# Optimization experiments

Measured on AMD Instinct MI355X. Metric: run time of the kernel, lower is better.

Reference implementation:

```python
import jax, jax.numpy as jnp
import numpy as np

B, L, C_IN = 16, 512, 32
D_MODEL, D_STATE, D_CONV, EXPAND, PRED_LEN = 128, 16, 4, 2, 96
D_INNER = EXPAND * D_MODEL          # 256
DT_RANK = (D_MODEL + 15) // 16      # 8 (ceil(d_model/16), mamba_ssm default)


def setup_inputs() -> dict:
    key = jax.random.key(0)
    ks = jax.random.split(key, 14)
    f32 = jnp.float32
    nrm = lambda k, shape, sc: jax.random.normal(k, shape, f32) * sc
    inp = {
        "x": jax.random.normal(ks[0], (B, L, C_IN), f32),
        # input_proj: Linear(enc_in, d_model)
        "W_in": nrm(ks[1], (C_IN, D_MODEL), C_IN ** -0.5),
        "b_in": jnp.zeros((D_MODEL,), f32),
        # Mamba in_proj: Linear(d_model, 2*d_inner, bias=False)
        "W_inproj": nrm(ks[2], (D_MODEL, 2 * D_INNER), D_MODEL ** -0.5),
        # depthwise causal conv1d (d_inner, d_conv) + bias
        "conv_w": nrm(ks[3], (D_INNER, D_CONV), D_CONV ** -0.5),
        "conv_b": jnp.zeros((D_INNER,), f32),
        # x_proj: Linear(d_inner, dt_rank + 2*d_state, bias=False)
        "W_xproj": nrm(ks[4], (D_INNER, DT_RANK + 2 * D_STATE), D_INNER ** -0.5),
        # dt_proj: Linear(dt_rank, d_inner) with bias init so softplus(bias) ~ 1e-3..1e-1
        "W_dt": nrm(ks[5], (DT_RANK, D_INNER), DT_RANK ** -0.5),
        "b_dt": jax.random.uniform(ks[6], (D_INNER,), f32, minval=-6.0, maxval=-3.0),
        # S4D-real A init: A = -exp(A_log), A_log = log(1..d_state)
        "A_log": jnp.log(jnp.tile(jnp.arange(1, D_STATE + 1, dtype=f32), (D_INNER, 1))),
        "D": jnp.ones((D_INNER,), f32),
        # Mamba out_proj: Linear(d_inner, d_model, bias=False)
        "W_out": nrm(ks[7], (D_INNER, D_MODEL), D_INNER ** -0.5),
        # output_proj: Linear(d_model*seq_len, pred_len*enc_in)
        "W_outproj": nrm(ks[8], (D_MODEL * L, PRED_LEN * C_IN), (D_MODEL * L) ** -0.5),
        "b_outproj": jnp.zeros((PRED_LEN * C_IN,), f32),
    }
    return inp


def _mamba_forward(x, W_in, b_in, W_inproj, conv_w, conv_b, W_xproj,
                   W_dt, b_dt, A_log, D, W_out, W_outproj, b_outproj):
    Bb, Ll, Cc = x.shape
    d_inner, d_conv = conv_w.shape
    d_state = A_log.shape[1]
    dt_rank = W_dt.shape[0]

    h = x @ W_in + b_in                                  # (B,L,d_model)
    xz = h @ W_inproj                                    # (B,L,2*d_inner)
    u, z = jnp.split(xz, 2, axis=-1)                     # each (B,L,d_inner)

    # causal depthwise conv1d along L
    uc = jnp.transpose(u, (0, 2, 1))                     # (B,d_inner,L)
    kern = conv_w[:, None, :]                            # (d_inner,1,d_conv)
    uc = jax.lax.conv_general_dilated(
        uc, kern, window_strides=(1,), padding=[(d_conv - 1, 0)],
        dimension_numbers=("NCH", "OIH", "NCH"), feature_group_count=d_inner)
    u = jax.nn.silu(jnp.transpose(uc, (0, 2, 1)) + conv_b)   # (B,L,d_inner)

    # input-dependent dt, B, C
    xdbc = u @ W_xproj                                   # (B,L,dt_rank+2*d_state)
    dt = jax.nn.softplus(xdbc[..., :dt_rank] @ W_dt + b_dt)  # (B,L,d_inner)
    Bm = xdbc[..., dt_rank:dt_rank + d_state]            # (B,L,d_state)
    Cm = xdbc[..., dt_rank + d_state:]                   # (B,L,d_state)

    A = -jnp.exp(A_log)                                  # (d_inner,d_state)
    dA = jnp.exp(jnp.einsum('bld,dn->bldn', dt, A))      # discretized A
    dBu = jnp.einsum('bld,bln,bld->bldn', dt, Bm, u)     # discretized B*u

    def step(hstate, inputs):
        dA_t, dBu_t, C_t = inputs                        # (B,d,n),(B,d,n),(B,n)
        hstate = dA_t * hstate + dBu_t
        y_t = jnp.einsum('bdn,bn->bd', hstate, C_t)
        return hstate, y_t

    h0 = jnp.zeros((Bb, d_inner, d_state), u.dtype)
    _, ys = jax.lax.scan(step, h0, (jnp.moveaxis(dA, 1, 0),
                                    jnp.moveaxis(dBu, 1, 0),
                                    jnp.moveaxis(Cm, 1, 0)))
    y = jnp.moveaxis(ys, 0, 1) + u * D                   # (B,L,d_inner)
    y = y * jax.nn.silu(z)                               # gating
    m_out = y @ W_out                                    # (B,L,d_model)

    flat = m_out.reshape(Bb, -1)                         # (B, L*d_model)
    pred = flat @ W_outproj + b_outproj                  # (B, pred_len*enc_in)
    return pred.reshape(Bb, W_outproj.shape[1] // Cc, Cc)


def reference(x, W_in, b_in, W_inproj, conv_w, conv_b, W_xproj,
              W_dt, b_dt, A_log, D, W_out, W_outproj, b_outproj):
    return _mamba_forward(x, W_in, b_in, W_inproj, conv_w, conv_b, W_xproj,
                          W_dt, b_dt, A_log, D, W_out, W_outproj, b_outproj)
```

## Files before the change

### kernel.cpp

```cpp
#include <hip/hip_runtime.h>
#include <math.h>

#define NB 16
#define LL 512
#define CIN 32
#define DM 128
#define DS 16
#define DI 256
#define DTR 8
#define NCOL 3072
#define KTOT 65536
#define ROWS 8192
#define CH 64
#define CLEN 8
#define KC 512
#define KS 128
#define OUTSZ 49152

typedef float f32x2 __attribute__((ext_vector_type(2)));

__device__ __forceinline__ float sigmoidf_(float x){ return 1.f/(1.f+expf(-x)); }
__device__ __forceinline__ float softplusf_(float x){ return (x > 20.f) ? x : log1pf(expf(x)); }

__global__ void __launch_bounds__(256) k_A(
    const float* __restrict__ x, const float* __restrict__ W_in,
    const float* __restrict__ b_in, const float* __restrict__ W_ip,
    const float* __restrict__ cw, const float* __restrict__ cb,
    float* __restrict__ u, float* __restrict__ z) {
  __shared__ float xs[11][32];
  __shared__ float hs[11][128];
  __shared__ float up[11][256];
  int t = threadIdx.x;
  int b  = blockIdx.x >> 6;
  int lt = blockIdx.x & 63;
  int l0 = lt * 8;
  for (int i=t; i<11*32; i+=256) {
    int r = i >> 5, c = i & 31;
    int li = l0 - 3 + r;
    xs[r][c] = (li >= 0) ? x[((b<<9)+li)*CIN + c] : 0.f;
  }
  __syncthreads();
  for (int i=t; i<11*128; i+=256) {
    int r = i >> 7, c = i & 127;
    float acc = b_in[c];
    #pragma unroll
    for (int k=0;k<CIN;k++) acc = fmaf(xs[r][k], W_in[k*DM+c], acc);
    hs[r][c] = acc;
  }
  __syncthreads();
  {
    int c0 = (t & 63)*4;
    int r0 = (t >> 6)*3;
    bool has2 = (r0+2 < 11);
    float acc[3][4] = {};
    for (int k=0;k<DM;k++) {
      float4 w = *(const float4*)(W_ip + k*512 + c0);
      float h0 = hs[r0][k], h1 = hs[r0+1][k];
      float h2 = has2 ? hs[r0+2][k] : 0.f;
      acc[0][0]=fmaf(h0,w.x,acc[0][0]); acc[0][1]=fmaf(h0,w.y,acc[0][1]);
      acc[0][2]=fmaf(h0,w.z,acc[0][2]); acc[0][3]=fmaf(h0,w.w,acc[0][3]);
      acc[1][0]=fmaf(h1,w.x,acc[1][0]); acc[1][1]=fmaf(h1,w.y,acc[1][1]);
      acc[1][2]=fmaf(h1,w.z,acc[1][2]); acc[1][3]=fmaf(h1,w.w,acc[1][3]);
      acc[2][0]=fmaf(h2,w.x,acc[2][0]); acc[2][1]=fmaf(h2,w.y,acc[2][1]);
      acc[2][2]=fmaf(h2,w.z,acc[2][2]); acc[2][3]=fmaf(h2,w.w,acc[2][3]);
    }
    *(float4*)&up[r0  ][c0] = make_float4(acc[0][0],acc[0][1],acc[0][2],acc[0][3]);
    *(float4*)&up[r0+1][c0] = make_float4(acc[1][0],acc[1][1],acc[1][2],acc[1][3]);
    if (has2)
      *(float4*)&up[r0+2][c0] = make_float4(acc[2][0],acc[2][1],acc[2][2],acc[2][3]);
  }
  {
    int c0 = (t & 63)*4;
    int r0 = (t >> 6)*2;
    float acc[2][4] = {};
    for (int k=0;k<DM;k++) {
      float4 w = *(const float4*)(W_ip + k*512 + 256 + c0);
      float h0 = hs[3+r0][k], h1 = hs[3+r0+1][k];
      acc[0][0]=fmaf(h0,w.x,acc[0][0]); acc[0][1]=fmaf(h0,w.y,acc[0][1]);
      acc[0][2]=fmaf(h0,w.z,acc[0][2]); acc[0][3]=fmaf(h0,w.w,acc[0][3]);
      acc[1][0]=fmaf(h1,w.x,acc[1][0]); acc[1][1]=fmaf(h1,w.y,acc[1][1]);
      acc[1][2]=fmaf(h1,w.z,acc[1][2]); acc[1][3]=fmaf(h1,w.w,acc[1][3]);
    }
    #pragma unroll
    for (int i=0;i<2;i++) {
      int gr = (b<<9) + l0 + r0 + i;
      *(float4*)(z + gr*DI + c0) =
        make_float4(acc[i][0],acc[i][1],acc[i][2],acc[i][3]);
    }
  }
  __syncthreads();
  for (int i=t; i<8*256; i+=256) {
    int r = i >> 8, d = i & 255;
    float s = cb[d];
    #pragma unroll
    for (int j=0;j<4;j++) {
      int li = l0 + r - 3 + j;
      if (li >= 0) s = fmaf(cw[d*4+j], up[r+j][d], s);
    }
    int gr = (b<<9) + l0 + r;
    u[gr*DI + d] = s * sigmoidf_(s);
  }
}

__global__ void __launch_bounds__(256) k_scan1(
    const float* __restrict__ u, const float* __restrict__ W_xp,
    const float* __restrict__ Wdt, const float* __restrict__ bdt,
    const float* __restrict__ A_log,
    float* __restrict__ Hc, float* __restrict__ Sdt) {
  __shared__ float us[CLEN][256];
  __shared__ float xl[CLEN][24];
  int t = threadIdx.x;
  int b = blockIdx.x >> 6, c = blockIdx.x & 63, d = t;
  int l0 = c * CLEN;
  for (int i=t; i<CLEN*64; i+=256) {
    int r = i >> 6, q = i & 63;
    *(float4*)&us[r][q*4] = *(const float4*)&u[(((b<<9)+l0+r)<<8) + q*4];
  }
  __syncthreads();
  for (int i=t; i<CLEN*24; i+=256) {
    int r = i / 24, cc = i - r*24;
    float acc = 0.f;
    #pragma unroll 8
    for (int k4=0;k4<64;k4++) {
      float4 uv = *(const float4*)&us[r][k4*4];
      acc = fmaf(uv.x, W_xp[(k4*4+0)*40+cc], acc);
      acc = fmaf(uv.y, W_xp[(k4*4+1)*40+cc], acc);
      acc = fmaf(uv.z, W_xp[(k4*4+2)*40+cc], acc);
      acc = fmaf(uv.w, W_xp[(k4*4+3)*40+cc], acc);
    }
    xl[r][cc] = acc;
  }
  __syncthreads();
  float A[16], hsv[16];
  #pragma unroll
  for (int n=0;n<16;n++){ A[n] = -expf(A_log[d*16+n]); hsv[n]=0.f; }
  float wdt[DTR];
  #pragma unroll
  for (int j=0;j<DTR;j++) wdt[j] = Wdt[j*DI+d];
  float bdtv = bdt[d];
  float sdt = 0.f;
  for (int l=0;l<CLEN;++l) {
    float acc = bdtv;
    #pragma unroll
    for (int j=0;j<DTR;j++) acc = fmaf(xl[l][j], wdt[j], acc);
    float dtv = softplusf_(acc);
    sdt += dtv;
    float du = dtv * us[l][d];
    #pragma unroll
    for (int n=0;n<16;n++) {
      float a = expf(dtv*A[n]);
      hsv[n] = fmaf(a, hsv[n], du * xl[l][DTR+n]);
    }
  }
  int bd = (b<<8) + d;
  int base = (bd*CH + c)*16;
  #pragma unroll
  for (int n=0;n<16;n++) Hc[base+n] = hsv[n];
  Sdt[bd*CH + c] = sdt;
}

__global__ void k_scan2(const float* __restrict__ A_log, const float* __restrict__ Hc,
                        const float* __restrict__ Sdt, float* __restrict__ Hst) {
  int idx = blockIdx.x*256 + threadIdx.x;
  int n  = idx & 15;
  int bd = idx >> 4;
  int d  = bd & 255;
  float A = -expf(A_log[d*16+n]);
  float hs = 0.f;
  int base = bd*CH*16;
  for (int c=0;c<CH;c++) {
    Hst[base + c*16 + n] = hs;
    float sdt = Sdt[bd*CH + c];
    hs = fmaf(expf(A*sdt), hs, Hc[base + c*16 + n]);
  }
}

__global__ void __launch_bounds__(256) k_scan3(
    const float* __restrict__ u, const float* __restrict__ z,
    const float* __restrict__ W_xp, const float* __restrict__ Wdt,
    const float* __restrict__ bdt, const float* __restrict__ A_log,
    const float* __restrict__ Dp, const float* __restrict__ Hst,
    const float* __restrict__ W_out, float* __restrict__ mo) {
  __shared__ float us[CLEN][256];
  __shared__ float ym[CLEN][256];
  __shared__ float xl[CLEN][40];
  int t = threadIdx.x;
  int b = blockIdx.x >> 6, c = blockIdx.x & 63, d = t;
  int l0 = c * CLEN;
  for (int i=t; i<CLEN*64; i+=256) {
    int r = i >> 6, q = i & 63;
    *(float4*)&us[r][q*4] = *(const float4*)&u[(((b<<9)+l0+r)<<8) + q*4];
  }
  __syncthreads();
  for (int i=t; i<CLEN*40; i+=256) {
    int r = i / 40, cc = i - r*40;
    float acc = 0.f;
    #pragma unroll 8
    for (int k4=0;k4<64;k4++) {
      float4 uv = *(const float4*)&us[r][k4*4];
      acc = fmaf(uv.x, W_xp[(k4*4+0)*40+cc], acc);
      acc = fmaf(uv.y, W_xp[(k4*4+1)*40+cc], acc);
      acc = fmaf(uv.z, W_xp[(k4*4+2)*40+cc], acc);
      acc = fmaf(uv.w, W_xp[(k4*4+3)*40+cc], acc);
    }
    xl[r][cc] = acc;
  }
  __syncthreads();
  int bd = (b<<8) + d;
  int base = (bd*CH + c)*16;
  float A[16], hsv[16];
  #pragma unroll
  for (int n=0;n<16;n++){ A[n] = -expf(A_log[d*16+n]); hsv[n] = Hst[base+n]; }
  float wdt[DTR];
  #pragma unroll
  for (int j=0;j<DTR;j++) wdt[j] = Wdt[j*DI+d];
  float bdtv = bdt[d];
  float Dv = Dp[d];
  for (int l=0;l<CLEN;++l) {
    int row = (b<<9) + l0 + l;
    float acc = bdtv;
    #pragma unroll
    for (int j=0;j<DTR;j++) acc = fmaf(xl[l][j], wdt[j], acc);
    float dtv = softplusf_(acc);
    float uv = us[l][d];
    float zv = z[(row<<8) + d];
    float du = dtv * uv;
    float y = 0.f;
    #pragma unroll
    for (int n=0;n<16;n++) {
      float a = expf(dtv*A[n]);
      hsv[n] = fmaf(a, hsv[n], du * xl[l][DTR+n]);
      y = fmaf(hsv[n], xl[l][DTR+DS+n], y);
    }
    y = fmaf(uv, Dv, y);
    ym[l][d] = y * (zv * sigmoidf_(zv));
  }
  __syncthreads();
  int cc = t & 127;
  int rg = (t >> 7) * 4;
  float acc[4] = {};
  for (int k4=0;k4<64;k4++) {
    float w0 = W_out[(k4*4+0)*DM+cc];
    float w1 = W_out[(k4*4+1)*DM+cc];
    float w2 = W_out[(k4*4+2)*DM+cc];
    float w3 = W_out[(k4*4+3)*DM+cc];
    #pragma unroll
    for (int o=0;o<4;o++) {
      float4 yv = *(const float4*)&ym[rg+o][k4*4];
      acc[o] = fmaf(yv.w, w3, fmaf(yv.z, w2, fmaf(yv.y, w1, fmaf(yv.x, w0, acc[o]))));
    }
  }
  #pragma unroll
  for (int o=0;o<4;o++) mo[((b<<9)+l0+rg+o)*DM + cc] = acc[o];
}

__global__ void __launch_bounds__(256) k_final(
    const float* __restrict__ flat, const float* __restrict__ W,
    float* __restrict__ part) {
  __shared__ float lds[KC][16];
  int t = threadIdx.x;
  int n0 = blockIdx.x * 512;
  int k0 = blockIdx.y * KC;
  for (int i = t; i < 16*(KC/4); i += 256) {
    int bb  = i & 15;
    int kk4 = i >> 4;
    float4 v = *(const float4*)(flat + bb*KTOT + k0 + kk4*4);
    lds[kk4*4+0][bb] = v.x; lds[kk4*4+1][bb] = v.y;
    lds[kk4*4+2][bb] = v.z; lds[kk4*4+3][bb] = v.w;
  }
  __syncthreads();
  int c0 = n0 + t*2;
  float2 acc[16];
  #pragma unroll
  for (int b=0;b<16;b++) acc[b] = make_float2(0.f,0.f);
  const float* Wp = W + (size_t)k0*NCOL + c0;
  for (int kk=0; kk<KC; kk+=4) {
    f32x2 w0 = __builtin_nontemporal_load((const f32x2*)(Wp + (size_t)(kk+0)*NCOL));
    f32x2 w1 = __builtin_nontemporal_load((const f32x2*)(Wp + (size_t)(kk+1)*NCOL));
    f32x2 w2 = __builtin_nontemporal_load((const f32x2*)(Wp + (size_t)(kk+2)*NCOL));
    f32x2 w3 = __builtin_nontemporal_load((const f32x2*)(Wp + (size_t)(kk+3)*NCOL));
    const float4* f0 = (const float4*)&lds[kk+0][0];
    const float4* f1 = (const float4*)&lds[kk+1][0];
    const float4* f2 = (const float4*)&lds[kk+2][0];
    const float4* f3 = (const float4*)&lds[kk+3][0];
    #pragma unroll
    for (int q=0;q<4;q++) {
      float4 fa = f0[q], fb = f1[q], fc = f2[q], fd = f3[q];
      float fs0[4] = {fa.x,fa.y,fa.z,fa.w};
      float fs1[4] = {fb.x,fb.y,fb.z,fb.w};
      float fs2[4] = {fc.x,fc.y,fc.z,fc.w};
      float fs3[4] = {fd.x,fd.y,fd.z,fd.w};
      #pragma unroll
      for (int j=0;j<4;j++) {
        int b = q*4+j;
        acc[b].x=fmaf(fs0[j],w0.x,acc[b].x); acc[b].y=fmaf(fs0[j],w0.y,acc[b].y);
        acc[b].x=fmaf(fs1[j],w1.x,acc[b].x); acc[b].y=fmaf(fs1[j],w1.y,acc[b].y);
        acc[b].x=fmaf(fs2[j],w2.x,acc[b].x); acc[b].y=fmaf(fs2[j],w2.y,acc[b].y);
        acc[b].x=fmaf(fs3[j],w3.x,acc[b].x); acc[b].y=fmaf(fs3[j],w3.y,acc[b].y);
      }
    }
  }
  float* p = part + (size_t)blockIdx.y*OUTSZ;
  #pragma unroll
  for (int b=0;b<16;b++) {
    f32x2 v; v.x = acc[b].x; v.y = acc[b].y;
    __builtin_nontemporal_store(v, (f32x2*)(p + b*NCOL + c0));
  }
}

__global__ void k_reduce(const float* __restrict__ part, const float* __restrict__ bias,
                         float* __restrict__ out) {
  int idx = blockIdx.x*256 + threadIdx.x;
  float acc = bias[idx % NCOL];
  #pragma unroll 8
  for (int s=0;s<KS;s++)
    acc += __builtin_nontemporal_load(part + (size_t)s*OUTSZ + idx);
  out[idx] = acc;
}

extern "C" void kernel_launch(void* const* d_in, const int* in_sizes, int n_in,
                              void* d_out, int out_size, void* d_ws, size_t ws_size,
                              hipStream_t stream) {
  const float* x        = (const float*)d_in[0];
  const float* W_in     = (const float*)d_in[1];
  const float* b_in     = (const float*)d_in[2];
  const float* W_inproj = (const float*)d_in[3];
  const float* conv_w   = (const float*)d_in[4];
  const float* conv_b   = (const float*)d_in[5];
  const float* W_xproj  = (const float*)d_in[6];
  const float* W_dt     = (const float*)d_in[7];
  const float* b_dt     = (const float*)d_in[8];
  const float* A_log    = (const float*)d_in[9];
  const float* Dp       = (const float*)d_in[10];
  const float* W_out    = (const float*)d_in[11];
  const float* W_outproj= (const float*)d_in[12];
  const float* b_outproj= (const float*)d_in[13];
  float* out = (float*)d_out;
  float* ws  = (float*)d_ws;

  float* u    = ws;
  float* z    = ws + 2097152;
  float* Hc   = ws + 4194304;
  float* Sdt  = ws + 8388608;
  float* Hst  = ws + 8650752;
  float* mo   = ws + 12845056;
  float* part = ws + 13893632;

  k_A     <<<1024, 256, 0, stream>>>(x, W_in, b_in, W_inproj, conv_w, conv_b, u, z);
  k_scan1 <<<1024, 256, 0, stream>>>(u, W_xproj, W_dt, b_dt, A_log, Hc, Sdt);
  k_scan2 <<<256,  256, 0, stream>>>(A_log, Hc, Sdt, Hst);
  k_scan3 <<<1024, 256, 0, stream>>>(u, z, W_xproj, W_dt, b_dt, A_log, Dp, Hst, W_out, mo);
  k_final <<<dim3(6, KS), 256, 0, stream>>>(mo, W_outproj, part);
  k_reduce<<<192,  256, 0, stream>>>(part, b_outproj, out);
}
```

Before: 289.8 us.

## Factor x_proj into its own kernel and vectorize in_proj LDS reads

```diff
diff --git a/kernel.cpp b/kernel.cpp
--- a/kernel.cpp
+++ b/kernel.cpp
@@ -53,16 +53,23 @@
     int r0 = (t >> 6)*3;
     bool has2 = (r0+2 < 11);
     float acc[3][4] = {};
-    for (int k=0;k<DM;k++) {
-      float4 w = *(const float4*)(W_ip + k*512 + c0);
-      float h0 = hs[r0][k], h1 = hs[r0+1][k];
-      float h2 = has2 ? hs[r0+2][k] : 0.f;
-      acc[0][0]=fmaf(h0,w.x,acc[0][0]); acc[0][1]=fmaf(h0,w.y,acc[0][1]);
-      acc[0][2]=fmaf(h0,w.z,acc[0][2]); acc[0][3]=fmaf(h0,w.w,acc[0][3]);
-      acc[1][0]=fmaf(h1,w.x,acc[1][0]); acc[1][1]=fmaf(h1,w.y,acc[1][1]);
-      acc[1][2]=fmaf(h1,w.z,acc[1][2]); acc[1][3]=fmaf(h1,w.w,acc[1][3]);
-      acc[2][0]=fmaf(h2,w.x,acc[2][0]); acc[2][1]=fmaf(h2,w.y,acc[2][1]);
-      acc[2][2]=fmaf(h2,w.z,acc[2][2]); acc[2][3]=fmaf(h2,w.w,acc[2][3]);
+    for (int k4=0;k4<32;k4++) {
+      float4 h0v = *(const float4*)&hs[r0][k4*4];
+      float4 h1v = *(const float4*)&hs[r0+1][k4*4];
+      float4 h2v = has2 ? *(const float4*)&hs[r0+2][k4*4] : make_float4(0.f,0.f,0.f,0.f);
+      float h0a[4]={h0v.x,h0v.y,h0v.z,h0v.w};
+      float h1a[4]={h1v.x,h1v.y,h1v.z,h1v.w};
+      float h2a[4]={h2v.x,h2v.y,h2v.z,h2v.w};
+      #pragma unroll
+      for (int j=0;j<4;j++) {
+        float4 w = *(const float4*)(W_ip + (k4*4+j)*512 + c0);
+        acc[0][0]=fmaf(h0a[j],w.x,acc[0][0]); acc[0][1]=fmaf(h0a[j],w.y,acc[0][1]);
+        acc[0][2]=fmaf(h0a[j],w.z,acc[0][2]); acc[0][3]=fmaf(h0a[j],w.w,acc[0][3]);
+        acc[1][0]=fmaf(h1a[j],w.x,acc[1][0]); acc[1][1]=fmaf(h1a[j],w.y,acc[1][1]);
+        acc[1][2]=fmaf(h1a[j],w.z,acc[1][2]); acc[1][3]=fmaf(h1a[j],w.w,acc[1][3]);
+        acc[2][0]=fmaf(h2a[j],w.x,acc[2][0]); acc[2][1]=fmaf(h2a[j],w.y,acc[2][1]);
+        acc[2][2]=fmaf(h2a[j],w.z,acc[2][2]); acc[2][3]=fmaf(h2a[j],w.w,acc[2][3]);
+      }
     }
     *(float4*)&up[r0  ][c0] = make_float4(acc[0][0],acc[0][1],acc[0][2],acc[0][3]);
     *(float4*)&up[r0+1][c0] = make_float4(acc[1][0],acc[1][1],acc[1][2],acc[1][3]);
@@ -73,13 +80,19 @@
     int c0 = (t & 63)*4;
     int r0 = (t >> 6)*2;
     float acc[2][4] = {};
-    for (int k=0;k<DM;k++) {
-      float4 w = *(const float4*)(W_ip + k*512 + 256 + c0);
-      float h0 = hs[3+r0][k], h1 = hs[3+r0+1][k];
-      acc[0][0]=fmaf(h0,w.x,acc[0][0]); acc[0][1]=fmaf(h0,w.y,acc[0][1]);
-      acc[0][2]=fmaf(h0,w.z,acc[0][2]); acc[0][3]=fmaf(h0,w.w,acc[0][3]);
-      acc[1][0]=fmaf(h1,w.x,acc[1][0]); acc[1][1]=fmaf(h1,w.y,acc[1][1]);
-      acc[1][2]=fmaf(h1,w.z,acc[1][2]); acc[1][3]=fmaf(h1,w.w,acc[1][3]);
+    for (int k4=0;k4<32;k4++) {
+      float4 h0v = *(const float4*)&hs[3+r0][k4*4];
+      float4 h1v = *(const float4*)&hs[3+r0+1][k4*4];
+      float h0a[4]={h0v.x,h0v.y,h0v.z,h0v.w};
+      float h1a[4]={h1v.x,h1v.y,h1v.z,h1v.w};
+      #pragma unroll
+      for (int j=0;j<4;j++) {
+        float4 w = *(const float4*)(W_ip + (k4*4+j)*512 + 256 + c0);
+        acc[0][0]=fmaf(h0a[j],w.x,acc[0][0]); acc[0][1]=fmaf(h0a[j],w.y,acc[0][1]);
+        acc[0][2]=fmaf(h0a[j],w.z,acc[0][2]); acc[0][3]=fmaf(h0a[j],w.w,acc[0][3]);
+        acc[1][0]=fmaf(h1a[j],w.x,acc[1][0]); acc[1][1]=fmaf(h1a[j],w.y,acc[1][1]);
+        acc[1][2]=fmaf(h1a[j],w.z,acc[1][2]); acc[1][3]=fmaf(h1a[j],w.w,acc[1][3]);
+      }
     }
     #pragma unroll
     for (int i=0;i<2;i++) {
@@ -102,34 +115,44 @@
   }
 }
 
+__global__ void __launch_bounds__(256) k_xproj(
+    const float* __restrict__ u, const float* __restrict__ W_xp,
+    float* __restrict__ xdbc) {
+  __shared__ float Wt[40][260];
+  int t = threadIdx.x;
+  for (int i=t; i<256*40; i+=256) {
+    int k = i / 40, c = i - k*40;
+    Wt[c][k] = W_xp[i];
+  }
+  __syncthreads();
+  int idx = blockIdx.x*256 + t;
+  int r = idx / 40, c = idx - r*40;
+  const float4* ur4 = (const float4*)(u + r*DI);
+  const float4* wc4 = (const float4*)&Wt[c][0];
+  float acc = 0.f;
+  #pragma unroll 8
+  for (int k4=0;k4<64;k4++) {
+    float4 uv = ur4[k4];
+    float4 wv = wc4[k4];
+    acc = fmaf(uv.x, wv.x, acc);
+    acc = fmaf(uv.y, wv.y, acc);
+    acc = fmaf(uv.z, wv.z, acc);
+    acc = fmaf(uv.w, wv.w, acc);
+  }
+  xdbc[idx] = acc;
+}
+
 __global__ void __launch_bounds__(256) k_scan1(
-    const float* __restrict__ u, const float* __restrict__ W_xp,
+    const float* __restrict__ u, const float* __restrict__ xdbc,
     const float* __restrict__ Wdt, const float* __restrict__ bdt,
     const float* __restrict__ A_log,
     float* __restrict__ Hc, float* __restrict__ Sdt) {
-  __shared__ float us[CLEN][256];
-  __shared__ float xl[CLEN][24];
+  __shared__ float xl[CLEN][40];
   int t = threadIdx.x;
   int b = blockIdx.x >> 6, c = blockIdx.x & 63, d = t;
   int l0 = c * CLEN;
-  for (int i=t; i<CLEN*64; i+=256) {
-    int r = i >> 6, q = i & 63;
-    *(float4*)&us[r][q*4] = *(const float4*)&u[(((b<<9)+l0+r)<<8) + q*4];
-  }
-  __syncthreads();
-  for (int i=t; i<CLEN*24; i+=256) {
-    int r = i / 24, cc = i - r*24;
-    float acc = 0.f;
-    #pragma unroll 8
-    for (int k4=0;k4<64;k4++) {
-      float4 uv = *(const float4*)&us[r][k4*4];
-      acc = fmaf(uv.x, W_xp[(k4*4+0)*40+cc], acc);
-      acc = fmaf(uv.y, W_xp[(k4*4+1)*40+cc], acc);
-      acc = fmaf(uv.z, W_xp[(k4*4+2)*40+cc], acc);
-      acc = fmaf(uv.w, W_xp[(k4*4+3)*40+cc], acc);
-    }
-    xl[r][cc] = acc;
-  }
+  int row0 = (b<<9) + l0;
+  for (int i=t; i<CLEN*40; i+=256) xl[i/40][i%40] = xdbc[row0*40 + i];
   __syncthreads();
   float A[16], hsv[16];
   #pragma unroll
@@ -145,7 +168,7 @@
     for (int j=0;j<DTR;j++) acc = fmaf(xl[l][j], wdt[j], acc);
     float dtv = softplusf_(acc);
     sdt += dtv;
-    float du = dtv * us[l][d];
+    float du = dtv * u[((row0+l)<<8) + d];
     #pragma unroll
     for (int n=0;n<16;n++) {
       float a = expf(dtv*A[n]);
@@ -177,34 +200,17 @@
 
 __global__ void __launch_bounds__(256) k_scan3(
     const float* __restrict__ u, const float* __restrict__ z,
-    const float* __restrict__ W_xp, const float* __restrict__ Wdt,
+    const float* __restrict__ xdbc, const float* __restrict__ Wdt,
     const float* __restrict__ bdt, const float* __restrict__ A_log,
     const float* __restrict__ Dp, const float* __restrict__ Hst,
     const float* __restrict__ W_out, float* __restrict__ mo) {
-  __shared__ float us[CLEN][256];
   __shared__ float ym[CLEN][256];
   __shared__ float xl[CLEN][40];
   int t = threadIdx.x;
   int b = blockIdx.x >> 6, c = blockIdx.x & 63, d = t;
   int l0 = c * CLEN;
-  for (int i=t; i<CLEN*64; i+=256) {
-    int r = i >> 6, q = i & 63;
-    *(float4*)&us[r][q*4] = *(const float4*)&u[(((b<<9)+l0+r)<<8) + q*4];
-  }
-  __syncthreads();
-  for (int i=t; i<CLEN*40; i+=256) {
-    int r = i / 40, cc = i - r*40;
-    float acc = 0.f;
-    #pragma unroll 8
-    for (int k4=0;k4<64;k4++) {
-      float4 uv = *(const float4*)&us[r][k4*4];
-      acc = fmaf(uv.x, W_xp[(k4*4+0)*40+cc], acc);
-      acc = fmaf(uv.y, W_xp[(k4*4+1)*40+cc], acc);
-      acc = fmaf(uv.z, W_xp[(k4*4+2)*40+cc], acc);
-      acc = fmaf(uv.w, W_xp[(k4*4+3)*40+cc], acc);
-    }
-    xl[r][cc] = acc;
-  }
+  int row0 = (b<<9) + l0;
+  for (int i=t; i<CLEN*40; i+=256) xl[i/40][i%40] = xdbc[row0*40 + i];
   __syncthreads();
   int bd = (b<<8) + d;
   int base = (bd*CH + c)*16;
@@ -217,12 +223,12 @@
   float bdtv = bdt[d];
   float Dv = Dp[d];
   for (int l=0;l<CLEN;++l) {
-    int row = (b<<9) + l0 + l;
+    int row = row0 + l;
     float acc = bdtv;
     #pragma unroll
     for (int j=0;j<DTR;j++) acc = fmaf(xl[l][j], wdt[j], acc);
     float dtv = softplusf_(acc);
-    float uv = us[l][d];
+    float uv = u[(row<<8) + d];
     float zv = z[(row<<8) + d];
     float du = dtv * uv;
     float y = 0.f;
@@ -251,7 +257,7 @@
     }
   }
   #pragma unroll
-  for (int o=0;o<4;o++) mo[((b<<9)+l0+rg+o)*DM + cc] = acc[o];
+  for (int o=0;o<4;o++) mo[(row0+rg+o)*DM + cc] = acc[o];
 }
 
 __global__ void __launch_bounds__(256) k_final(
@@ -340,16 +346,18 @@
 
   float* u    = ws;
   float* z    = ws + 2097152;
-  float* Hc   = ws + 4194304;
-  float* Sdt  = ws + 8388608;
-  float* Hst  = ws + 8650752;
-  float* mo   = ws + 12845056;
-  float* part = ws + 13893632;
+  float* xdbc = ws + 4194304;
+  float* Hc   = ws + 4521984;
+  float* Sdt  = ws + 8716288;
+  float* Hst  = ws + 8978432;
+  float* mo   = ws + 13172736;
+  float* part = ws + 14221312;
 
   k_A     <<<1024, 256, 0, stream>>>(x, W_in, b_in, W_inproj, conv_w, conv_b, u, z);
-  k_scan1 <<<1024, 256, 0, stream>>>(u, W_xproj, W_dt, b_dt, A_log, Hc, Sdt);
+  k_xproj <<<1280, 256, 0, stream>>>(u, W_xproj, xdbc);
+  k_scan1 <<<1024, 256, 0, stream>>>(u, xdbc, W_dt, b_dt, A_log, Hc, Sdt);
   k_scan2 <<<256,  256, 0, stream>>>(A_log, Hc, Sdt, Hst);
-  k_scan3 <<<1024, 256, 0, stream>>>(u, z, W_xproj, W_dt, b_dt, A_log, Dp, Hst, W_out, mo);
+  k_scan3 <<<1024, 256, 0, stream>>>(u, z, xdbc, W_dt, b_dt, A_log, Dp, Hst, W_out, mo);
   k_final <<<dim3(6, KS), 256, 0, stream>>>(mo, W_outproj, part);
   k_reduce<<<192,  256, 0, stream>>>(part, b_outproj, out);
 }
```

Result: no change. 290.4 us (+0.2%).
